# Performance work log

Measured on AMD Instinct MI355X. Metric: run time of the kernel, lower is better.

Reference implementation:

```python
import jax, jax.numpy as jnp
import numpy as np

K = 3        # ksize
S = 2        # stride_1
P = K // 2   # padding
SCALE = 10.0 # softmax_scale


def conv1x1(x, w, bias):
    # x: [bs, C, D, H, W], w: [O, C] (1x1x1 Conv3d), bias: [O]
    return jnp.einsum('bcdhw,oc->bodhw', x, w) + bias[None, :, None, None, None]


def _win_idx(n_in):
    n_out = (n_in + 2 * P - K) // S + 1
    idx = (jnp.arange(n_out) * S)[:, None] + jnp.arange(K)  # [n_out, K]
    return idx, n_out


def unfold2d(x):
    # x: [bs, C, H, W] -> patches [bs, C, nH, nW, K, K] (torch Unfold semantics, zero pad)
    bs, C, H, W = x.shape
    xp = jnp.pad(x, ((0, 0), (0, 0), (P, P), (P, P)))
    ri, nH = _win_idx(H)
    ci, nW = _win_idx(W)
    return xp[:, :, ri[:, None, :, None], ci[None, :, None, :]]


def fold2d(pat, H, W):
    # pat: [bs, C, nH, nW, K, K] -> [bs, C, H, W] via overlap-add (torch Fold)
    bs, C, nH, nW, _, _ = pat.shape
    ri, _ = _win_idx(H)
    ci, _ = _win_idx(W)
    out = jnp.zeros((bs, C, H + 2 * P, W + 2 * P), pat.dtype)
    out = out.at[:, :, ri[:, None, :, None], ci[None, :, None, :]].add(pat)
    return out[:, :, P:P + H, P:P + W]


def _patches_flat(x2d):
    # x2d: [bs, Ci, H, W] -> ([bs*L, Ci*K*K], nH, nW)  matching torch's
    # unfold -> view(bs,Ci,K,K,L) -> permute(0,4,1,2,3) -> reshape layout
    pat = unfold2d(x2d)                      # [bs, Ci, nH, nW, K, K]
    bs, Ci, nH, nW = pat.shape[:4]
    flat = jnp.transpose(pat, (0, 2, 3, 1, 4, 5)).reshape(bs * nH * nW, Ci * K * K)
    return flat, nH, nW


def salsa_one(b_one, g_w, g_b, th_w, th_b, ph_w, ph_b, W_w, W_b):
    bs, C, D, H, W = b_one.shape
    Ci = g_w.shape[0]
    b1 = conv1x1(b_one, g_w, g_b)    # query source
    b2 = conv1x1(b_one, th_w, th_b)  # value source
    b3 = conv1x1(b_one, ph_w, ph_b)  # key source
    mid = D // 2

    q, nH, nW = _patches_flat(b1[:, :, mid])   # [bs*L, Ci*K*K]
    v, _, _ = _patches_flat(b2[:, :, mid])
    kq, _, _ = _patches_flat(b3[:, :, mid])

    att = jax.nn.softmax(SCALE * (q @ kq.T), axis=1)  # [bs*L, bs*L]
    zi = att @ v                                      # [bs*L, Ci*K*K]

    pat = jnp.transpose(zi.reshape(bs, nH, nW, Ci, K, K), (0, 3, 1, 2, 4, 5))
    zi2 = fold2d(pat, H, W)                           # [bs, Ci, H, W]
    # overlap-count normalization: fold(unfold(ones))
    mask = fold2d(unfold2d(jnp.ones((bs, Ci, H, W), b_one.dtype)), H, W)
    zi2 = zi2 / mask

    zi5 = jnp.broadcast_to(zi2[:, :, None], (bs, Ci, D, H, W))
    return b_one + conv1x1(zi5, W_w, W_b)


def setup_inputs() -> dict:
    key = jax.random.key(0)
    ks = jax.random.split(key, 9)
    C, Ci = 64, 16
    b = jax.random.normal(ks[0], (2, 1, C, 8, 160, 160), dtype=jnp.float32)
    mk = lambda k, shp: jax.random.normal(k, shp, dtype=jnp.float32) * 0.05
    return {
        'b': b,
        'g_w': mk(ks[1], (Ci, C)), 'g_b': mk(ks[2], (Ci,)),
        'theta_w': mk(ks[3], (Ci, C)), 'theta_b': mk(ks[4], (Ci,)),
        'phi_w': mk(ks[5], (Ci, C)), 'phi_b': mk(ks[6], (Ci,)),
        'W_w': mk(ks[7], (C, Ci)), 'W_b': mk(ks[8], (C,)),
    }


def reference(b, g_w, g_b, theta_w, theta_b, phi_w, phi_b, W_w, W_b):
    f = lambda x: salsa_one(x, g_w, g_b, theta_w, theta_b, phi_w, phi_b, W_w, W_b)
    return jax.vmap(f)(b)
```

## Files before the change

### kernel.cpp

```cpp
#include <hip/hip_runtime.h>


#define NPIX 25600
#define LOG2E10 14.42695040888963f
#define TAU 0.75f

typedef float floatx16 __attribute__((ext_vector_type(16)));
typedef short short8 __attribute__((ext_vector_type(8)));

__device__ inline unsigned short f2bf(float x) {
    union { __bf16 h; unsigned short u; } v;
    v.h = (__bf16)x;
    return v.u;
}
__device__ inline float bf2f(unsigned short u) {
    union { unsigned int u; float f; } v; v.u = ((unsigned int)u) << 16;
    return v.f;
}

__global__ __launch_bounds__(256) void k_proj(
    const float* __restrict__ b,
    const float* __restrict__ gw, const float* __restrict__ gb,
    const float* __restrict__ thw, const float* __restrict__ thb,
    const float* __restrict__ phw, const float* __restrict__ phb,
    float* __restrict__ P3) {
    __shared__ float Wt[3 * 64 * 16];
    __shared__ float Bl[48];
    __shared__ float red[2][48][64];
    int tid = threadIdx.x;
    int g = blockIdx.y;
    int px = tid & 63;
    int cq = tid >> 6;
    int pix = blockIdx.x * 64 + px;

    for (int i = tid; i < 1024; i += 256) {
        int o = i & 15, c = i >> 4;
        Wt[(0 * 64 + c) * 16 + o] = gw[o * 64 + c];
        Wt[(1 * 64 + c) * 16 + o] = phw[o * 64 + c];
        Wt[(2 * 64 + c) * 16 + o] = thw[o * 64 + c];
    }
    if (tid < 16) { Bl[tid] = gb[tid]; Bl[16 + tid] = phb[tid]; Bl[32 + tid] = thb[tid]; }
    __syncthreads();

    float acc[48];
#pragma unroll
    for (int o = 0; o < 48; o++) acc[o] = 0.f;
    const float* bp = b + (size_t)g * 64 * 8 * NPIX + (size_t)4 * NPIX + pix;
#pragma unroll
    for (int i = 0; i < 16; i++) {
        int c = cq * 16 + i;
        float xv = bp[(size_t)c * 8 * NPIX];
#pragma unroll
        for (int s = 0; s < 3; s++) {
            const float* wp = &Wt[(s * 64 + c) * 16];
#pragma unroll
            for (int o = 0; o < 16; o++)
                acc[s * 16 + o] += wp[o] * xv;
        }
    }
    if (cq >= 2) {
#pragma unroll
        for (int o = 0; o < 48; o++) red[cq - 2][o][px] = acc[o];
    }
    __syncthreads();
    if (cq < 2) {
#pragma unroll
        for (int o = 0; o < 48; o++) acc[o] += red[cq][o][px];
    }
    __syncthreads();
    if (cq == 1) {
#pragma unroll
        for (int o = 0; o < 48; o++) red[0][o][px] = acc[o];
    }
    __syncthreads();
    if (cq == 0) {
#pragma unroll
        for (int o = 0; o < 48; o++)
            P3[(size_t)(g * 48 + o) * NPIX + pix] = acc[o] + red[0][o][px] + Bl[o];
    }
}

__global__ void k_unfold_qk(const float* __restrict__ P3, unsigned short* __restrict__ Pat) {
    int idx = blockIdx.x * 256 + threadIdx.x;
    int j = idx % 18;
    int rest = idx / 18;
    int l = rest % 6400;
    int gs = rest / 6400;
    int s = gs & 1, g = gs >> 1;
    int oh = l / 80, ow = l % 80;
    int h0 = oh * 2 - 1, w0 = ow * 2 - 1;
    const float* src = P3 + (size_t)(g * 48 + s * 16) * NPIX;
    short8 outv;
#pragma unroll
    for (int e = 0; e < 8; e++) {
        int f = j * 8 + e;
        int ci = f / 9;
        int rem = f - ci * 9;
        int kr = rem / 3;
        int kc = rem - kr * 3;
        int h = h0 + kr, w = w0 + kc;
        float v = 0.f;
        if (h >= 0 && h < 160 && w >= 0 && w < 160)
            v = src[(size_t)ci * NPIX + h * 160 + w];
        outv[e] = (short)f2bf(v);
    }
    *(short8*)(Pat + ((size_t)gs * 6400 + l) * 144 + j * 8) = outv;
}

__global__ void k_unfold_v(const float* __restrict__ P3, unsigned short* __restrict__ VT) {
    int idx = blockIdx.x * 256 + threadIdx.x;
    int lc = idx % 800;
    int f = (idx / 800) % 144;
    int g = idx / (800 * 144);
    int l0 = lc * 8;
    int oh = l0 / 80, ow0 = l0 - oh * 80;
    int ci = f / 9;
    int rem = f - ci * 9;
    int kr = rem / 3;
    int kc = rem - kr * 3;
    int h = oh * 2 + kr - 1;
    short8 outv;
    if (h >= 0 && h < 160) {
        const float* row = P3 + (size_t)(g * 48 + 32 + ci) * NPIX + h * 160;
#pragma unroll
        for (int e = 0; e < 8; e++) {
            int w = (ow0 + e) * 2 + kc - 1;
            float v = (w >= 0 && w < 160) ? row[w] : 0.f;
            outv[e] = (short)f2bf(v);
        }
    } else {
#pragma unroll
        for (int e = 0; e < 8; e++) outv[e] = 0;
    }
    *(short8*)(VT + ((size_t)g * 144 + f) * 6400 + l0) = outv;
}

__global__ __launch_bounds__(256, 2) void k_attn(
    const unsigned short* __restrict__ PatQK, const unsigned short* __restrict__ VT,
    float* __restrict__ ml, unsigned short* __restrict__ Opart,
    int nsplit, int kps) {
    __shared__ unsigned short Ks[64 * 156];
    __shared__ unsigned short Vs[160 * 76];
    __shared__ unsigned short Pl[4 * 32 * 76];

    int tid = threadIdx.x;
    int lane = tid & 63;
    int w = tid >> 6;
    int l31 = lane & 31;
    int h5 = lane >> 5;
    int split = blockIdx.y, g = blockIdx.z;
    int q = blockIdx.x * 128 + w * 32 + l31;
    int nIter = kps >> 6;

    const unsigned short* Qg = PatQK + ((size_t)g * 2 + 0) * 6400 * 144;
    const unsigned short* Kg = PatQK + ((size_t)g * 2 + 1) * 6400 * 144 + (size_t)split * kps * 144;
    const unsigned short* Vg = VT + (size_t)g * 144 * 6400 + split * kps;

    short8 qf[9];
#pragma unroll
    for (int fs = 0; fs < 9; fs++)
        qf[fs] = *(const short8*)(Qg + (size_t)q * 144 + fs * 16 + h5 * 8);

    floatx16 O[5];
#pragma unroll
    for (int i = 0; i < 5; i++) O[i] = (floatx16)0.f;
    float m = -1e30f, lsum = 0.f;

    unsigned short* Plw = Pl + w * (32 * 76);

    short8 stg[9];
    {
#pragma unroll
        for (int j = 0; j < 9; j++) {
            int c = tid + 256 * j;
            if (c < 1152) {
                int row = c / 18, col = c - row * 18;
                stg[j] = *(const short8*)(Kg + row * 144 + col * 8);
            } else {
                int vv = c - 1152;
                int f = vv >> 3, col = vv & 7;
                stg[j] = *(const short8*)(Vg + (size_t)f * 6400 + col * 8);
            }
        }
#pragma unroll
        for (int j = 0; j < 9; j++) {
            int c = tid + 256 * j;
            if (c < 1152) {
                int row = c / 18, col = c - row * 18;
                *(short8*)&Ks[row * 156 + col * 8] = stg[j];
            } else {
                int vv = c - 1152;
                int f = vv >> 3, col = vv & 7;
                *(short8*)&Vs[f * 76 + col * 8] = stg[j];
            }
        }
    }

    for (int it = 0; it < nIter; it++) {
        __syncthreads();

        if (it + 1 < nIter) {
            const unsigned short* Kt = Kg + (it + 1) * 64 * 144;
            const unsigned short* Vt = Vg + (it + 1) * 64;
#pragma unroll
            for (int j = 0; j < 9; j++) {
                int c = tid + 256 * j;
                if (c < 1152) {
                    int row = c / 18, col = c - row * 18;
                    stg[j] = *(const short8*)(Kt + row * 144 + col * 8);
                } else {
                    int vv = c - 1152;
                    int f = vv >> 3, col = vv & 7;
                    stg[j] = *(const short8*)(Vt + (size_t)f * 6400 + col * 8);
                }
            }
        }

        floatx16 S0 = (floatx16)0.f, S1 = (floatx16)0.f;
#pragma unroll
        for (int fs = 0; fs < 9; fs++) {
            short8 a0 = *(const short8*)&Ks[l31 * 156 + fs * 16 + h5 * 8];
            short8 a1 = *(const short8*)&Ks[(32 + l31) * 156 + fs * 16 + h5 * 8];
            S0 = __builtin_amdgcn_mfma_f32_32x32x16_bf16(a0, qf[fs], S0, 0, 0, 0);
            S1 = __builtin_amdgcn_mfma_f32_32x32x16_bf16(a1, qf[fs], S1, 0, 0, 0);
        }

        float mx[8];
#pragma unroll
        for (int i = 0; i < 8; i++)
            mx[i] = fmaxf(fmaxf(S0[2 * i], S0[2 * i + 1]), fmaxf(S1[2 * i], S1[2 * i + 1]));
        float mt = fmaxf(fmaxf(fmaxf(mx[0], mx[1]), fmaxf(mx[2], mx[3])),
                         fmaxf(fmaxf(mx[4], mx[5]), fmaxf(mx[6], mx[7])));
        mt = fmaxf(mt, __shfl_xor(mt, 32, 64));
        bool upd = mt > m + TAU;
        float mnew = upd ? mt : m;
        float alpha = upd ? exp2f(LOG2E10 * (m - mnew)) : 1.f;
        float nb = LOG2E10 * mnew;
        float pa = 0.f, pb2 = 0.f, pc = 0.f, pd = 0.f;
#pragma unroll
        for (int r = 0; r < 16; r += 2) {
            S0[r]     = exp2f(fmaf(LOG2E10, S0[r],     -nb));
            S0[r + 1] = exp2f(fmaf(LOG2E10, S0[r + 1], -nb));
            S1[r]     = exp2f(fmaf(LOG2E10, S1[r],     -nb));
            S1[r + 1] = exp2f(fmaf(LOG2E10, S1[r + 1], -nb));
            pa += S0[r]; pb2 += S0[r + 1]; pc += S1[r]; pd += S1[r + 1];
        }
        float ps = (pa + pb2) + (pc + pd);
        ps += __shfl_xor(ps, 32, 64);
        lsum = lsum * alpha + ps;
        m = mnew;
        if (__any(alpha < 1.f)) {
#pragma unroll
            for (int t5 = 0; t5 < 5; t5++)
#pragma unroll
                for (int r = 0; r < 16; r++) O[t5][r] *= alpha;
        }

#pragma unroll
        for (int rg = 0; rg < 4; rg++) {
            ushort4 w0, w1;
            w0.x = f2bf(S0[4 * rg + 0]); w0.y = f2bf(S0[4 * rg + 1]);
            w0.z = f2bf(S0[4 * rg + 2]); w0.w = f2bf(S0[4 * rg + 3]);
            w1.x = f2bf(S1[4 * rg + 0]); w1.y = f2bf(S1[4 * rg + 1]);
            w1.z = f2bf(S1[4 * rg + 2]); w1.w = f2bf(S1[4 * rg + 3]);
            *(ushort4*)&Plw[l31 * 76 + rg * 8 + h5 * 4] = w0;
            *(ushort4*)&Plw[l31 * 76 + 32 + rg * 8 + h5 * 4] = w1;
        }

#pragma unroll
        for (int ks = 0; ks < 4; ks++) {
            short8 pb = *(const short8*)&Plw[l31 * 76 + ks * 16 + h5 * 8];
#pragma unroll
            for (int ft = 0; ft < 5; ft++) {
                short8 va = *(const short8*)&Vs[(ft * 32 + l31) * 76 + ks * 16 + h5 * 8];
                O[ft] = __builtin_amdgcn_mfma_f32_32x32x16_bf16(va, pb, O[ft], 0, 0, 0);
            }
        }

        __syncthreads();
        if (it + 1 < nIter) {
#pragma unroll
            for (int j = 0; j < 9; j++) {
                int c = tid + 256 * j;
                if (c < 1152) {
                    int row = c / 18, col = c - row * 18;
                    *(short8*)&Ks[row * 156 + col * 8] = stg[j];
                } else {
                    int vv = c - 1152;
                    int f = vv >> 3, col = vv & 7;
                    *(short8*)&Vs[f * 76 + col * 8] = stg[j];
                }
            }
        }
    }

    if (h5 == 0)
        ((float2*)ml)[((size_t)g * nsplit + split) * 6400 + q] = make_float2(m, lsum);

    unsigned short* Og = Opart + (((size_t)g * nsplit + split) * 6400 + q) * 144;
#pragma unroll
    for (int ft = 0; ft < 5; ft++)
#pragma unroll
        for (int rg = 0; rg < 4; rg++) {
            int f = ft * 32 + rg * 8 + h5 * 4;
            if (f < 144) {
                ushort4 st;
                st.x = f2bf(O[ft][4 * rg + 0]); st.y = f2bf(O[ft][4 * rg + 1]);
                st.z = f2bf(O[ft][4 * rg + 2]); st.w = f2bf(O[ft][4 * rg + 3]);
                *(ushort4*)(Og + f) = st;
            }
        }
}

__global__ void k_merge(const float* __restrict__ mlp, const unsigned short* __restrict__ Opart,
                        float* __restrict__ Zi, int nsplit) {
    int idx = blockIdx.x * 256 + threadIdx.x;
    int fg = idx % 36;
    int q = (idx / 36) % 6400;
    int g = idx / (36 * 6400);
    const float2* ml2 = (const float2*)mlp;
    float2 s[5];
    float ms = -1e30f;
#pragma unroll
    for (int k = 0; k < 5; k++) {
        s[k] = (k < nsplit) ? ml2[((size_t)g * nsplit + k) * 6400 + q]
                            : make_float2(-1e30f, 0.f);
        ms = fmaxf(ms, s[k].x);
    }
    float wgt[5], denom = 0.f;
#pragma unroll
    for (int k = 0; k < 5; k++) {
        wgt[k] = exp2f(LOG2E10 * (s[k].x - ms));
        denom += wgt[k] * s[k].y;
    }
    float inv = 1.f / denom;
    float a0 = 0.f, a1 = 0.f, a2 = 0.f, a3 = 0.f;
#pragma unroll
    for (int k = 0; k < 5; k++) {
        if (k < nsplit) {
            ushort4 u = *(const ushort4*)(Opart + (((size_t)g * nsplit + k) * 6400 + q) * 144 + fg * 4);
            a0 += wgt[k] * bf2f(u.x); a1 += wgt[k] * bf2f(u.y);
            a2 += wgt[k] * bf2f(u.z); a3 += wgt[k] * bf2f(u.w);
        }
    }
    float4 out = make_float4(a0 * inv, a1 * inv, a2 * inv, a3 * inv);
    *(float4*)(Zi + ((size_t)g * 6400 + q) * 144 + fg * 4) = out;
}

__global__ void k_fold(const float* __restrict__ Zi, float* __restrict__ zi2) {
    int idx = blockIdx.x * 256 + threadIdx.x;
    int pix = idx % NPIX;
    int ci = (idx / NPIX) & 15;
    int g = idx / (16 * NPIX);
    int h = pix / 160, w = pix % 160;
    int ohs[2], krs[2], nh = 0;
#pragma unroll
    for (int kr = 0; kr < 3; kr++) {
        int t = h + 1 - kr;
        if (t >= 0 && (t & 1) == 0 && (t >> 1) < 80) { ohs[nh] = t >> 1; krs[nh] = kr; nh++; }
    }
    int ows[2], kcs[2], nw = 0;
#pragma unroll
    for (int kc = 0; kc < 3; kc++) {
        int t = w + 1 - kc;
        if (t >= 0 && (t & 1) == 0 && (t >> 1) < 80) { ows[nw] = t >> 1; kcs[nw] = kc; nw++; }
    }
    float sm = 0.f;
    for (int a = 0; a < nh; a++)
        for (int bb = 0; bb < nw; bb++) {
            int l = ohs[a] * 80 + ows[bb];
            int f = ci * 9 + krs[a] * 3 + kcs[bb];
            sm += Zi[((size_t)g * 6400 + l) * 144 + f];
        }
    zi2[idx] = sm / (float)(nh * nw);
}

__global__ void k_final(const float* __restrict__ b, const float* __restrict__ zi2,
                        const float* __restrict__ Ww, const float* __restrict__ Wb,
                        float* __restrict__ out) {
    __shared__ float z[16 * 64];
    __shared__ float Wl[64 * 16];
    __shared__ float Bl[64];
    int tid = threadIdx.x;
    int g = blockIdx.y;
    int pxb = blockIdx.x * 64;
    for (int i = tid; i < 1024; i += 256) {
        int ci = i >> 6, px = i & 63;
        z[i] = zi2[(size_t)(g * 16 + ci) * NPIX + pxb + px];
        Wl[i] = Ww[i];
    }
    if (tid < 64) Bl[tid] = Wb[tid];
    __syncthreads();

    int px4 = tid & 15;
    int cg = tid >> 4;
    float acc[4][4];
#pragma unroll
    for (int c4 = 0; c4 < 4; c4++) {
        float bv = Bl[cg + 16 * c4];
#pragma unroll
        for (int j = 0; j < 4; j++) acc[c4][j] = bv;
    }
#pragma unroll
    for (int ci = 0; ci < 16; ci++) {
        float zv[4];
#pragma unroll
        for (int j = 0; j < 4; j++) zv[j] = z[ci * 64 + px4 * 4 + j];
#pragma unroll
        for (int c4 = 0; c4 < 4; c4++) {
            float wv = Wl[(cg + 16 * c4) * 16 + ci];
#pragma unroll
            for (int j = 0; j < 4; j++) acc[c4][j] += wv * zv[j];
        }
    }
    for (int d = 0; d < 8; d++) {
#pragma unroll
        for (int c4 = 0; c4 < 4; c4++) {
            int c = cg + 16 * c4;
            size_t base = ((size_t)(g * 64 + c) * 8 + d) * NPIX + pxb + px4 * 4;
            float4 bv = *(const float4*)(b + base);
            float4 ov = make_float4(bv.x + acc[c4][0], bv.y + acc[c4][1],
                                    bv.z + acc[c4][2], bv.w + acc[c4][3]);
            *(float4*)(out + base) = ov;
        }
    }
}

extern "C" void kernel_launch(void* const* d_in, const int* in_sizes, int n_in,
                              void* d_out, int out_size, void* d_ws, size_t ws_size,
                              hipStream_t stream) {
    const float* b   = (const float*)d_in[0];
    const float* gw  = (const float*)d_in[1];
    const float* gb  = (const float*)d_in[2];
    const float* thw = (const float*)d_in[3];
    const float* thb = (const float*)d_in[4];
    const float* phw = (const float*)d_in[5];
    const float* phb = (const float*)d_in[6];
    const float* Ww  = (const float*)d_in[7];
    const float* Wb  = (const float*)d_in[8];
    float* out = (float*)d_out;
    float* ws = (float*)d_ws;

    const size_t need5 = 30003200;
    int ns = (ws_size >= need5) ? 5 : 4;
    int kps = 6400 / ns;

    unsigned short* PatQK = (unsigned short*)ws;
    unsigned short* VT    = (unsigned short*)(ws + 1843200);
    float*          ml    = ws + 2764800;
    size_t off_P3 = 2764800 + (size_t)2 * ns * 6400 * 2;
    float*          P3    = ws + off_P3;
    unsigned short* Opart = (unsigned short*)(ws + off_P3);
    float*          Zi    = ws;
    float*          zi2   = ws + 1843200;

    k_proj<<<dim3(400, 2), 256, 0, stream>>>(b, gw, gb, thw, thb, phw, phb, P3);
    k_unfold_qk<<<dim3(1800), 256, 0, stream>>>(P3, PatQK);
    k_unfold_v<<<dim3(900), 256, 0, stream>>>(P3, VT);
    k_attn<<<dim3(50, ns, 2), 256, 0, stream>>>(PatQK, VT, ml, Opart, ns, kps);
    k_merge<<<dim3(1800), 256, 0, stream>>>(ml, Opart, Zi, ns);
    k_fold<<<dim3(3200), 256, 0, stream>>>(Zi, zi2);
    k_final<<<dim3(400, 2), 256, 0, stream>>>(b, zi2, Ww, Wb, out);
}
```

Baseline: 343.3 us.

## Shrink attention LDS footprint, alias P buffer onto K, allow ten KV splits

```diff
diff --git a/kernel.cpp b/kernel.cpp
--- a/kernel.cpp
+++ b/kernel.cpp
@@ -4,6 +4,12 @@
 #define NPIX 25600
 #define LOG2E10 14.42695040888963f
 #define TAU 0.75f
+
+#define KS_LD 146
+#define VS_LD 66
+#define PL_LD 66
+#define KS_SH (64 * KS_LD)
+#define VS_SH (160 * VS_LD)
 
 typedef float floatx16 __attribute__((ext_vector_type(16)));
 typedef short short8 __attribute__((ext_vector_type(8)));
@@ -139,9 +145,10 @@
     const unsigned short* __restrict__ PatQK, const unsigned short* __restrict__ VT,
     float* __restrict__ ml, unsigned short* __restrict__ Opart,
     int nsplit, int kps) {
-    __shared__ unsigned short Ks[64 * 156];
-    __shared__ unsigned short Vs[160 * 76];
-    __shared__ unsigned short Pl[4 * 32 * 76];
+    __shared__ unsigned short SM[KS_SH + VS_SH];
+    unsigned short* Ks = SM;
+    unsigned short* Vs = SM + KS_SH;
+    unsigned short* Pl = SM;
 
     int tid = threadIdx.x;
     int lane = tid & 63;
@@ -166,7 +173,9 @@
     for (int i = 0; i < 5; i++) O[i] = (floatx16)0.f;
     float m = -1e30f, lsum = 0.f;
 
-    unsigned short* Plw = Pl + w * (32 * 76);
+    unsigned short* Plw = Pl + w * (32 * PL_LD);
+
+    for (int i = tid; i < 16 * VS_LD; i += 256) Vs[144 * VS_LD + i] = 0;
 
     short8 stg[9];
     {
@@ -187,11 +196,11 @@
             int c = tid + 256 * j;
             if (c < 1152) {
                 int row = c / 18, col = c - row * 18;
-                *(short8*)&Ks[row * 156 + col * 8] = stg[j];
+                *(short8*)&Ks[row * KS_LD + col * 8] = stg[j];
             } else {
                 int vv = c - 1152;
                 int f = vv >> 3, col = vv & 7;
-                *(short8*)&Vs[f * 76 + col * 8] = stg[j];
+                *(short8*)&Vs[f * VS_LD + col * 8] = stg[j];
             }
         }
     }
@@ -219,8 +228,8 @@
         floatx16 S0 = (floatx16)0.f, S1 = (floatx16)0.f;
 #pragma unroll
         for (int fs = 0; fs < 9; fs++) {
-            short8 a0 = *(const short8*)&Ks[l31 * 156 + fs * 16 + h5 * 8];
-            short8 a1 = *(const short8*)&Ks[(32 + l31) * 156 + fs * 16 + h5 * 8];
+            short8 a0 = *(const short8*)&Ks[l31 * KS_LD + fs * 16 + h5 * 8];
+            short8 a1 = *(const short8*)&Ks[(32 + l31) * KS_LD + fs * 16 + h5 * 8];
             S0 = __builtin_amdgcn_mfma_f32_32x32x16_bf16(a0, qf[fs], S0, 0, 0, 0);
             S1 = __builtin_amdgcn_mfma_f32_32x32x16_bf16(a1, qf[fs], S1, 0, 0, 0);
         }
@@ -256,6 +265,8 @@
                 for (int r = 0; r < 16; r++) O[t5][r] *= alpha;
         }
 
+        __syncthreads();
+
 #pragma unroll
         for (int rg = 0; rg < 4; rg++) {
             ushort4 w0, w1;
@@ -263,32 +274,32 @@
             w0.z = f2bf(S0[4 * rg + 2]); w0.w = f2bf(S0[4 * rg + 3]);
             w1.x = f2bf(S1[4 * rg + 0]); w1.y = f2bf(S1[4 * rg + 1]);
             w1.z = f2bf(S1[4 * rg + 2]); w1.w = f2bf(S1[4 * rg + 3]);
-            *(ushort4*)&Plw[l31 * 76 + rg * 8 + h5 * 4] = w0;
-            *(ushort4*)&Plw[l31 * 76 + 32 + rg * 8 + h5 * 4] = w1;
+            *(ushort4*)&Plw[l31 * PL_LD + rg * 8 + h5 * 4] = w0;
+            *(ushort4*)&Plw[l31 * PL_LD + 32 + rg * 8 + h5 * 4] = w1;
         }
 
 #pragma unroll
         for (int ks = 0; ks < 4; ks++) {
-            short8 pb = *(const short8*)&Plw[l31 * 76 + ks * 16 + h5 * 8];
+            short8 pb = *(const short8*)&Plw[l31 * PL_LD + ks * 16 + h5 * 8];
 #pragma unroll
             for (int ft = 0; ft < 5; ft++) {
-                short8 va = *(const short8*)&Vs[(ft * 32 + l31) * 76 + ks * 16 + h5 * 8];
+                short8 va = *(const short8*)&Vs[(ft * 32 + l31) * VS_LD + ks * 16 + h5 * 8];
                 O[ft] = __builtin_amdgcn_mfma_f32_32x32x16_bf16(va, pb, O[ft], 0, 0, 0);
             }
         }
 
-        __syncthreads();
         if (it + 1 < nIter) {
+            __syncthreads();
 #pragma unroll
             for (int j = 0; j < 9; j++) {
                 int c = tid + 256 * j;
                 if (c < 1152) {
                     int row = c / 18, col = c - row * 18;
-                    *(short8*)&Ks[row * 156 + col * 8] = stg[j];
+                    *(short8*)&Ks[row * KS_LD + col * 8] = stg[j];
                 } else {
                     int vv = c - 1152;
                     int f = vv >> 3, col = vv & 7;
-                    *(short8*)&Vs[f * 76 + col * 8] = stg[j];
+                    *(short8*)&Vs[f * VS_LD + col * 8] = stg[j];
                 }
             }
         }
@@ -319,24 +330,24 @@
     int q = (idx / 36) % 6400;
     int g = idx / (36 * 6400);
     const float2* ml2 = (const float2*)mlp;
-    float2 s[5];
+    float2 s[10];
     float ms = -1e30f;
 #pragma unroll
-    for (int k = 0; k < 5; k++) {
+    for (int k = 0; k < 10; k++) {
         s[k] = (k < nsplit) ? ml2[((size_t)g * nsplit + k) * 6400 + q]
                             : make_float2(-1e30f, 0.f);
         ms = fmaxf(ms, s[k].x);
     }
-    float wgt[5], denom = 0.f;
-#pragma unroll
-    for (int k = 0; k < 5; k++) {
+    float wgt[10], denom = 0.f;
+#pragma unroll
+    for (int k = 0; k < 10; k++) {
         wgt[k] = exp2f(LOG2E10 * (s[k].x - ms));
         denom += wgt[k] * s[k].y;
     }
     float inv = 1.f / denom;
     float a0 = 0.f, a1 = 0.f, a2 = 0.f, a3 = 0.f;
 #pragma unroll
-    for (int k = 0; k < 5; k++) {
+    for (int k = 0; k < 10; k++) {
         if (k < nsplit) {
             ushort4 u = *(const ushort4*)(Opart + (((size_t)g * nsplit + k) * 6400 + q) * 144 + fg * 4);
             a0 += wgt[k] * bf2f(u.x); a1 += wgt[k] * bf2f(u.y);
@@ -441,8 +452,9 @@
     float* out = (float*)d_out;
     float* ws = (float*)d_ws;
 
-    const size_t need5 = 30003200;
-    int ns = (ws_size >= need5) ? 5 : 4;
+    const size_t need10 = 48947200;
+    const size_t need5  = 30003200;
+    int ns = (ws_size >= need10) ? 10 : (ws_size >= need5) ? 5 : 4;
     int kps = 6400 / ns;
 
     unsigned short* PatQK = (unsigned short*)ws;
```

Measured after the change: 523.9 us. 1.53x slower.

## Deepen K/V register prefetch to two tiles ahead with ping-pong staging

Applied to the files above, without the earlier changes.

```diff
diff --git a/kernel.cpp b/kernel.cpp
--- a/kernel.cpp
+++ b/kernel.cpp
@@ -168,18 +168,19 @@
 
     unsigned short* Plw = Pl + w * (32 * 76);
 
-    short8 stg[9];
+    short8 stgA[9], stgB[9];
+
     {
 #pragma unroll
         for (int j = 0; j < 9; j++) {
             int c = tid + 256 * j;
             if (c < 1152) {
                 int row = c / 18, col = c - row * 18;
-                stg[j] = *(const short8*)(Kg + row * 144 + col * 8);
+                stgA[j] = *(const short8*)(Kg + row * 144 + col * 8);
             } else {
                 int vv = c - 1152;
                 int f = vv >> 3, col = vv & 7;
-                stg[j] = *(const short8*)(Vg + (size_t)f * 6400 + col * 8);
+                stgA[j] = *(const short8*)(Vg + (size_t)f * 6400 + col * 8);
             }
         }
 #pragma unroll
@@ -187,31 +188,47 @@
             int c = tid + 256 * j;
             if (c < 1152) {
                 int row = c / 18, col = c - row * 18;
-                *(short8*)&Ks[row * 156 + col * 8] = stg[j];
+                *(short8*)&Ks[row * 156 + col * 8] = stgA[j];
             } else {
                 int vv = c - 1152;
                 int f = vv >> 3, col = vv & 7;
-                *(short8*)&Vs[f * 76 + col * 8] = stg[j];
-            }
-        }
-    }
-
-    for (int it = 0; it < nIter; it++) {
-        __syncthreads();
-
-        if (it + 1 < nIter) {
-            const unsigned short* Kt = Kg + (it + 1) * 64 * 144;
-            const unsigned short* Vt = Vg + (it + 1) * 64;
+                *(short8*)&Vs[f * 76 + col * 8] = stgA[j];
+            }
+        }
+        if (nIter > 1) {
+            const unsigned short* Kt = Kg + 64 * 144;
+            const unsigned short* Vt = Vg + 64;
 #pragma unroll
             for (int j = 0; j < 9; j++) {
                 int c = tid + 256 * j;
                 if (c < 1152) {
                     int row = c / 18, col = c - row * 18;
-                    stg[j] = *(const short8*)(Kt + row * 144 + col * 8);
+                    stgA[j] = *(const short8*)(Kt + row * 144 + col * 8);
                 } else {
                     int vv = c - 1152;
                     int f = vv >> 3, col = vv & 7;
-                    stg[j] = *(const short8*)(Vt + (size_t)f * 6400 + col * 8);
+                    stgA[j] = *(const short8*)(Vt + (size_t)f * 6400 + col * 8);
+                }
+            }
+        }
+    }
+
+    auto body = [&](int it, short8 (&sC)[9], short8 (&sN)[9]) {
+        __syncthreads();
+
+        if (it + 2 < nIter) {
+            const unsigned short* Kt = Kg + (it + 2) * 64 * 144;
+            const unsigned short* Vt = Vg + (it + 2) * 64;
+#pragma unroll
+            for (int j = 0; j < 9; j++) {
+                int c = tid + 256 * j;
+                if (c < 1152) {
+                    int row = c / 18, col = c - row * 18;
+                    sN[j] = *(const short8*)(Kt + row * 144 + col * 8);
+                } else {
+                    int vv = c - 1152;
+                    int f = vv >> 3, col = vv & 7;
+                    sN[j] = *(const short8*)(Vt + (size_t)f * 6400 + col * 8);
                 }
             }
         }
@@ -284,15 +301,22 @@
                 int c = tid + 256 * j;
                 if (c < 1152) {
                     int row = c / 18, col = c - row * 18;
-                    *(short8*)&Ks[row * 156 + col * 8] = stg[j];
+                    *(short8*)&Ks[row * 156 + col * 8] = sC[j];
                 } else {
                     int vv = c - 1152;
                     int f = vv >> 3, col = vv & 7;
-                    *(short8*)&Vs[f * 76 + col * 8] = stg[j];
+                    *(short8*)&Vs[f * 76 + col * 8] = sC[j];
                 }
             }
         }
-    }
+    };
+
+    int it = 0;
+    for (; it + 1 < nIter; it += 2) {
+        body(it, stgA, stgB);
+        body(it + 1, stgB, stgA);
+    }
+    if (it < nIter) body(it, stgA, stgB);
 
     if (h5 == 0)
         ((float2*)ml)[((size_t)g * nsplit + split) * 6400 + q] = make_float2(m, lsum);
```

Result: slower. 483.7 us (+40.9%).
